# Kernel tuning notes

Measured on AMD Instinct MI355X. Metric: run time of the kernel, lower is better.

## Reference

```python
import jax, jax.numpy as jnp
import numpy as np

MARGIN = 0.3
BIG = 10000.0  # sentinel used by the original when a gt/lt negative set is empty


def setup_inputs() -> dict:
    key = jax.random.key(0)
    k1, k2 = jax.random.split(key)
    inputs = jax.random.normal(k1, (4096, 256), dtype=jnp.float32)
    targets = jax.random.randint(k2, (4096,), 0, 4, dtype=jnp.int32)
    return {"inputs": inputs, "targets": targets}


def reference(inputs, targets):
    # Pairwise Euclidean distance matrix (n, n).
    sq = jnp.sum(inputs * inputs, axis=1)
    d2 = sq[:, None] + sq[None, :] - 2.0 * (inputs @ inputs.T)
    dist = jnp.sqrt(jnp.maximum(d2, 0.0))

    # mask[i, j] semantics from the torch code (rows of expand are `targets`):
    #   eq: targets[j] == targets[i]; gt: targets[j] > targets[i]; lt: targets[j] < targets[i]
    eq = targets[None, :] == targets[:, None]
    gt = targets[None, :] > targets[:, None]
    lt = targets[None, :] < targets[:, None]

    # Hardest positive: max distance over same-label columns (diag always eq -> non-empty).
    hard_ap = jnp.max(jnp.where(eq, dist, -jnp.inf), axis=1)
    # Hardest greater / less negatives: min distance, sentinel BIG when set empty.
    an_g = jnp.min(jnp.where(gt, dist, jnp.inf), axis=1)
    an_g = jnp.where(jnp.isinf(an_g), BIG, an_g)
    an_l = jnp.min(jnp.where(lt, dist, jnp.inf), axis=1)
    an_l = jnp.where(jnp.isinf(an_l), BIG, an_l)

    loss = jnp.mean(jax.nn.relu(hard_ap - jnp.abs(an_g - an_l) + MARGIN))
    # cnt: rows whose positive set is just the anchor itself
    cnt = jnp.sum(jnp.sum(eq, axis=1) == 1)
    return loss, dist, cnt
```

## Files before the change

kernel.cpp:

```cpp
#include <hip/hip_runtime.h>

#define N 4096
#define D 256
#define MARGIN 0.3f
#define BIG 10000.0f

typedef _Float16 f16x8 __attribute__((ext_vector_type(8)));
typedef _Float16 f16x4 __attribute__((ext_vector_type(4)));
typedef float floatx16 __attribute__((ext_vector_type(16)));

__device__ inline void atomicMaxFloatPos(float* a, float v) {
    atomicMax((int*)a, __float_as_int(v));
}
__device__ inline void atomicMinFloatPos(float* a, float v) {
    atomicMin((int*)a, __float_as_int(v));
}

__device__ inline void gl_lds16(const void* g, void* l) {
    __builtin_amdgcn_global_load_lds(
        (const __attribute__((address_space(1))) unsigned int*)g,
        (__attribute__((address_space(3))) unsigned int*)l, 16, 0, 0);
}

__global__ __launch_bounds__(256) void prep_kernel(const float* __restrict__ x,
                                                   float* __restrict__ sq,
                                                   _Float16* __restrict__ Xf,
                                                   float* ap, float* ang, float* anl) {
    const int wave = threadIdx.x >> 6, lane = threadIdx.x & 63;
    const int row = blockIdx.x * 4 + wave;
    const float4 v = *(const float4*)(x + (size_t)row * D + lane * 4);
    f16x4 h;
    h[0] = (_Float16)v.x; h[1] = (_Float16)v.y;
    h[2] = (_Float16)v.z; h[3] = (_Float16)v.w;
    *(f16x4*)(Xf + (size_t)row * D + lane * 4) = h;
    const float c0 = (float)h[0], c1 = (float)h[1], c2 = (float)h[2], c3 = (float)h[3];
    float s = c0 * c0 + c1 * c1 + c2 * c2 + c3 * c3;
    #pragma unroll
    for (int off = 32; off; off >>= 1) s += __shfl_down(s, off);
    if (lane == 0) sq[row] = s;
    if (threadIdx.x < 4) {
        const int i = blockIdx.x * 4 + threadIdx.x;
        ap[i] = 0.0f; ang[i] = BIG; anl[i] = BIG;
    }
}

__global__ __launch_bounds__(64) void dist_kernel(const _Float16* __restrict__ Xf,
                                                  const int* __restrict__ tgt,
                                                  const float* __restrict__ sq,
                                                  float* __restrict__ dist,
                                                  float* ap, float* ang, float* anl) {
    __shared__ _Float16 lds[8192];
    _Float16* ldsA = lds;
    _Float16* ldsB = lds + 4096;
    float*    ldsC = (float*)lds;

    const int lane = threadIdx.x;
    const int row0 = blockIdx.y * 64;
    const int col0 = blockIdx.x * 64;

    const int drow = lane >> 3;
    const int q    = (lane & 7) ^ drow;

    floatx16 acc[2][2];
    #pragma unroll
    for (int mt = 0; mt < 2; ++mt)
        #pragma unroll
        for (int nt = 0; nt < 2; ++nt)
            #pragma unroll
            for (int r = 0; r < 16; ++r) acc[mt][nt][r] = 0.0f;

    const int m0 = lane & 31;
    const int m1 = 32 + m0;

    for (int s = 0; s < 4; ++s) {
        const int k0 = s * 64;
        __asm__ volatile("s_waitcnt lgkmcnt(0)" ::: "memory");
        #pragma unroll
        for (int d = 0; d < 8; ++d) {
            const int r = d * 8 + drow;
            gl_lds16(Xf + (size_t)(row0 + r) * D + k0 + q * 8, ldsA + d * 512);
            gl_lds16(Xf + (size_t)(col0 + r) * D + k0 + q * 8, ldsB + d * 512);
        }
        __asm__ volatile("s_waitcnt vmcnt(0)" ::: "memory");

        #pragma unroll
        for (int ks = 0; ks < 4; ++ks) {
            const int lq = ks * 2 + (lane >> 5);
            f16x8 a0 = *(const f16x8*)(ldsA + m0 * 64 + ((lq ^ (m0 & 7)) << 3));
            f16x8 a1 = *(const f16x8*)(ldsA + m1 * 64 + ((lq ^ (m1 & 7)) << 3));
            f16x8 b0 = *(const f16x8*)(ldsB + m0 * 64 + ((lq ^ (m0 & 7)) << 3));
            f16x8 b1 = *(const f16x8*)(ldsB + m1 * 64 + ((lq ^ (m1 & 7)) << 3));
            acc[0][0] = __builtin_amdgcn_mfma_f32_32x32x16_f16(a0, b0, acc[0][0], 0, 0, 0);
            acc[0][1] = __builtin_amdgcn_mfma_f32_32x32x16_f16(a0, b1, acc[0][1], 0, 0, 0);
            acc[1][0] = __builtin_amdgcn_mfma_f32_32x32x16_f16(a1, b0, acc[1][0], 0, 0, 0);
            acc[1][1] = __builtin_amdgcn_mfma_f32_32x32x16_f16(a1, b1, acc[1][1], 0, 0, 0);
        }
        __asm__ volatile("" ::: "memory");
    }

    const int gc0 = col0 + m0, gc1 = col0 + 32 + m0;
    const float sqc0 = sq[gc0], sqc1 = sq[gc1];
    const int rl_base = 4 * (lane >> 5);

    #pragma unroll
    for (int mt = 0; mt < 2; ++mt) {
        #pragma unroll
        for (int r = 0; r < 16; ++r) {
            const int row_l = mt * 32 + (r & 3) + 8 * (r >> 2) + rl_base;
            const int grow  = row0 + row_l;
            const float sqi = sq[grow];
            const float d0 = sqrtf(fmaxf(sqi + sqc0 - 2.0f * acc[mt][0][r], 0.0f));
            const float d1 = sqrtf(fmaxf(sqi + sqc1 - 2.0f * acc[mt][1][r], 0.0f));
            dist[(size_t)grow * N + gc0] = d0;
            dist[(size_t)grow * N + gc1] = d1;
            const int sw = row_l & 15;
            ldsC[row_l * 64 + (((m0 >> 2) ^ sw) << 2) + (m0 & 3)] = d0;
            ldsC[row_l * 64 + ((((m0 + 32) >> 2) ^ sw) << 2) + (m0 & 3)] = d1;
        }
    }
    __asm__ volatile("s_waitcnt lgkmcnt(0)" ::: "memory");

    const int grow = row0 + lane;
    const int ti   = tgt[grow];
    float mx = 0.0f, mg = BIG, ml = BIG;
    #pragma unroll
    for (int j = 0; j < 16; ++j) {
        const int4  t4 = *(const int4*)&tgt[col0 + j * 4];
        const float4 d4 = *(const float4*)&ldsC[lane * 64 + ((j ^ (lane & 15)) << 2)];
        if (t4.x == ti) mx = fmaxf(mx, d4.x); else if (t4.x > ti) mg = fminf(mg, d4.x); else ml = fminf(ml, d4.x);
        if (t4.y == ti) mx = fmaxf(mx, d4.y); else if (t4.y > ti) mg = fminf(mg, d4.y); else ml = fminf(ml, d4.y);
        if (t4.z == ti) mx = fmaxf(mx, d4.z); else if (t4.z > ti) mg = fminf(mg, d4.z); else ml = fminf(ml, d4.z);
        if (t4.w == ti) mx = fmaxf(mx, d4.w); else if (t4.w > ti) mg = fminf(mg, d4.w); else ml = fminf(ml, d4.w);
    }
    atomicMaxFloatPos(&ap[grow], mx);
    atomicMinFloatPos(&ang[grow], mg);
    atomicMinFloatPos(&anl[grow], ml);
}

__global__ __launch_bounds__(1024) void finish_kernel(const float* __restrict__ ap,
                                                      const float* __restrict__ ang,
                                                      const float* __restrict__ anl,
                                                      const int* __restrict__ tgt,
                                                      float* __restrict__ out) {
    __shared__ int hist[4];
    __shared__ unsigned hsum[2][16];
    __shared__ float wsum[16];
    __shared__ int wcnt[16];
    const int tid = threadIdx.x, lane = tid & 63, wv = tid >> 6;

    const int4 t4 = *(const int4*)&tgt[tid * 4];
    int c[4] = {0, 0, 0, 0};
    c[t4.x & 3]++; c[t4.y & 3]++; c[t4.z & 3]++; c[t4.w & 3]++;
    unsigned p01 = (unsigned)c[0] | ((unsigned)c[1] << 16);
    unsigned p23 = (unsigned)c[2] | ((unsigned)c[3] << 16);
    #pragma unroll
    for (int off = 32; off; off >>= 1) {
        p01 += __shfl_down(p01, off);
        p23 += __shfl_down(p23, off);
    }
    if (lane == 0) { hsum[0][wv] = p01; hsum[1][wv] = p23; }
    __syncthreads();
    if (tid == 0) {
        unsigned a = 0, b = 0;
        for (int i = 0; i < 16; ++i) { a += hsum[0][i]; b += hsum[1][i]; }
        hist[0] = a & 0xFFFF; hist[1] = a >> 16;
        hist[2] = b & 0xFFFF; hist[3] = b >> 16;
    }
    __syncthreads();

    float term = 0.0f; int cc = 0;
    const int lab[4] = {t4.x & 3, t4.y & 3, t4.z & 3, t4.w & 3};
    #pragma unroll
    for (int j = 0; j < 4; ++j) {
        const int i = tid * 4 + j;
        term += fmaxf(ap[i] - fabsf(ang[i] - anl[i]) + MARGIN, 0.0f);
        cc += (hist[lab[j]] == 1) ? 1 : 0;
    }
    #pragma unroll
    for (int off = 32; off; off >>= 1) {
        term += __shfl_down(term, off);
        cc   += __shfl_down(cc, off);
    }
    if (lane == 0) { wsum[wv] = term; wcnt[wv] = cc; }
    __syncthreads();
    if (tid == 0) {
        float ls = 0.0f; int cs = 0;
        for (int i = 0; i < 16; ++i) { ls += wsum[i]; cs += wcnt[i]; }
        out[0] = ls * (1.0f / N);
        out[1 + (size_t)N * N] = (float)cs;
    }
}

extern "C" void kernel_launch(void* const* d_in, const int* in_sizes, int n_in,
                              void* d_out, int out_size, void* d_ws, size_t ws_size,
                              hipStream_t stream) {
    const float* x   = (const float*)d_in[0];
    const int*   tgt = (const int*)d_in[1];
    float* out = (float*)d_out;
    char*  ws  = (char*)d_ws;

    _Float16* Xf  = (_Float16*)ws;
    float*    sq  = (float*)(ws + 2097152);
    float*    ap  = sq + 4096;
    float*    ang = sq + 8192;
    float*    anl = sq + 12288;

    prep_kernel<<<N / 4, 256, 0, stream>>>(x, sq, Xf, ap, ang, anl);
    dim3 grid(N / 64, N / 64);
    dist_kernel<<<grid, 64, 0, stream>>>(Xf, tgt, sq, out + 1, ap, ang, anl);
    finish_kernel<<<1, 1024, 0, stream>>>(ap, ang, anl, tgt, out);
}
```

Measured before the change: 114.6 us.

## Double-buffer global-to-LDS tile loads in distance GEMM kernel

Splits the LDS staging area into two A/B buffer pairs and unrolls the four K-steps. The next K-slice's global_load_lds is issued before computing on the current one, using partial vmcnt waits. This overlaps global memory latency with MFMA work inside each single-wave block, which previously waited for every load before computing. In exchange, LDS per block doubles, which can lower the number of resident blocks per CU. Buffer reuse also relies on the LDS reads of the previous compute finishing before the next load overwrites them.

```diff
diff --git a/kernel.cpp b/kernel.cpp
--- a/kernel.cpp
+++ b/kernel.cpp
@@ -49,9 +49,11 @@
                                                   const float* __restrict__ sq,
                                                   float* __restrict__ dist,
                                                   float* ap, float* ang, float* anl) {
-    __shared__ _Float16 lds[8192];
-    _Float16* ldsA = lds;
-    _Float16* ldsB = lds + 4096;
+    __shared__ _Float16 lds[16384];
+    _Float16* A0 = lds;
+    _Float16* B0 = lds + 4096;
+    _Float16* A1 = lds + 8192;
+    _Float16* B1 = lds + 12288;
     float*    ldsC = (float*)lds;
 
     const int lane = threadIdx.x;
@@ -60,6 +62,38 @@
 
     const int drow = lane >> 3;
     const int q    = (lane & 7) ^ drow;
+    const _Float16* gA = Xf + (size_t)(row0 + drow) * D + q * 8;
+    const _Float16* gB = Xf + (size_t)(col0 + drow) * D + q * 8;
+
+    const int m0 = lane & 31;
+    const int m1 = 32 + m0;
+
+    #define ISSUE(k0, la, lb)                                             \
+        {                                                                 \
+            _Pragma("unroll")                                             \
+            for (int d = 0; d < 8; ++d) {                                 \
+                gl_lds16(gA + (size_t)d * 8 * D + (k0), (la) + d * 512);  \
+                gl_lds16(gB + (size_t)d * 8 * D + (k0), (lb) + d * 512);  \
+            }                                                             \
+        }
+
+    #define COMPUTE(la, lb)                                                            \
+        {                                                                              \
+            _Pragma("unroll")                                                          \
+            for (int ks = 0; ks < 4; ++ks) {                                           \
+                const int lq = ks * 2 + (lane >> 5);                                   \
+                f16x8 a0 = *(const f16x8*)((la) + m0 * 64 + ((lq ^ (m0 & 7)) << 3));   \
+                f16x8 a1 = *(const f16x8*)((la) + m1 * 64 + ((lq ^ (m1 & 7)) << 3));   \
+                f16x8 b0 = *(const f16x8*)((lb) + m0 * 64 + ((lq ^ (m0 & 7)) << 3));   \
+                f16x8 b1 = *(const f16x8*)((lb) + m1 * 64 + ((lq ^ (m1 & 7)) << 3));   \
+                acc[0][0] = __builtin_amdgcn_mfma_f32_32x32x16_f16(a0, b0, acc[0][0], 0, 0, 0); \
+                acc[0][1] = __builtin_amdgcn_mfma_f32_32x32x16_f16(a0, b1, acc[0][1], 0, 0, 0); \
+                acc[1][0] = __builtin_amdgcn_mfma_f32_32x32x16_f16(a1, b0, acc[1][0], 0, 0, 0); \
+                acc[1][1] = __builtin_amdgcn_mfma_f32_32x32x16_f16(a1, b1, acc[1][1], 0, 0, 0); \
+            }                                                                          \
+        }
+
+    ISSUE(0, A0, B0);
 
     floatx16 acc[2][2];
     #pragma unroll
@@ -69,34 +103,17 @@
             #pragma unroll
             for (int r = 0; r < 16; ++r) acc[mt][nt][r] = 0.0f;
 
-    const int m0 = lane & 31;
-    const int m1 = 32 + m0;
-
-    for (int s = 0; s < 4; ++s) {
-        const int k0 = s * 64;
-        __asm__ volatile("s_waitcnt lgkmcnt(0)" ::: "memory");
-        #pragma unroll
-        for (int d = 0; d < 8; ++d) {
-            const int r = d * 8 + drow;
-            gl_lds16(Xf + (size_t)(row0 + r) * D + k0 + q * 8, ldsA + d * 512);
-            gl_lds16(Xf + (size_t)(col0 + r) * D + k0 + q * 8, ldsB + d * 512);
-        }
-        __asm__ volatile("s_waitcnt vmcnt(0)" ::: "memory");
-
-        #pragma unroll
-        for (int ks = 0; ks < 4; ++ks) {
-            const int lq = ks * 2 + (lane >> 5);
-            f16x8 a0 = *(const f16x8*)(ldsA + m0 * 64 + ((lq ^ (m0 & 7)) << 3));
-            f16x8 a1 = *(const f16x8*)(ldsA + m1 * 64 + ((lq ^ (m1 & 7)) << 3));
-            f16x8 b0 = *(const f16x8*)(ldsB + m0 * 64 + ((lq ^ (m0 & 7)) << 3));
-            f16x8 b1 = *(const f16x8*)(ldsB + m1 * 64 + ((lq ^ (m1 & 7)) << 3));
-            acc[0][0] = __builtin_amdgcn_mfma_f32_32x32x16_f16(a0, b0, acc[0][0], 0, 0, 0);
-            acc[0][1] = __builtin_amdgcn_mfma_f32_32x32x16_f16(a0, b1, acc[0][1], 0, 0, 0);
-            acc[1][0] = __builtin_amdgcn_mfma_f32_32x32x16_f16(a1, b0, acc[1][0], 0, 0, 0);
-            acc[1][1] = __builtin_amdgcn_mfma_f32_32x32x16_f16(a1, b1, acc[1][1], 0, 0, 0);
-        }
-        __asm__ volatile("" ::: "memory");
-    }
+    ISSUE(64, A1, B1);
+    __asm__ volatile("s_waitcnt vmcnt(16)" ::: "memory");
+    COMPUTE(A0, B0);
+    ISSUE(128, A0, B0);
+    __asm__ volatile("s_waitcnt vmcnt(16)" ::: "memory");
+    COMPUTE(A1, B1);
+    ISSUE(192, A1, B1);
+    __asm__ volatile("s_waitcnt vmcnt(16)" ::: "memory");
+    COMPUTE(A0, B0);
+    __asm__ volatile("s_waitcnt vmcnt(0)" ::: "memory");
+    COMPUTE(A1, B1);
 
     const int gc0 = col0 + m0, gc1 = col0 + 32 + m0;
     const float sqc0 = sq[gc0], sqc1 = sq[gc1];
@@ -135,6 +152,8 @@
     atomicMaxFloatPos(&ap[grow], mx);
     atomicMinFloatPos(&ang[grow], mg);
     atomicMinFloatPos(&anl[grow], ml);
+    #undef ISSUE
+    #undef COMPUTE
 }
 
 __global__ __launch_bounds__(1024) void finish_kernel(const float* __restrict__ ap,
```

Result: slower. 131.1 us (+14.3%).

## Load MFMA operands directly from global, reduce per row via shuffles, fuse finish

Applied to the files above, without the earlier changes.

Drops the LDS staging of the A/B tiles and loads f16x8 operands straight from global memory into the MFMA inputs. The per-row max/min reduction now runs in registers with cross-lane shuffles and atomics, with no LDS round trip. The finish kernel is folded into the last block, found through a global atomic counter. This removes LDS traffic and one launch, but adds many shuffles and atomics per row, uncoalesced global loads, and a single-wave serial tail.

```diff
diff --git a/kernel.cpp b/kernel.cpp
--- a/kernel.cpp
+++ b/kernel.cpp
@@ -4,6 +4,7 @@
 #define D 256
 #define MARGIN 0.3f
 #define BIG 10000.0f
+#define NBLK 4096
 
 typedef _Float16 f16x8 __attribute__((ext_vector_type(8)));
 typedef _Float16 f16x4 __attribute__((ext_vector_type(4)));
@@ -16,16 +17,11 @@
     atomicMin((int*)a, __float_as_int(v));
 }
 
-__device__ inline void gl_lds16(const void* g, void* l) {
-    __builtin_amdgcn_global_load_lds(
-        (const __attribute__((address_space(1))) unsigned int*)g,
-        (__attribute__((address_space(3))) unsigned int*)l, 16, 0, 0);
-}
-
 __global__ __launch_bounds__(256) void prep_kernel(const float* __restrict__ x,
                                                    float* __restrict__ sq,
                                                    _Float16* __restrict__ Xf,
-                                                   float* ap, float* ang, float* anl) {
+                                                   float* ap, float* ang, float* anl,
+                                                   unsigned* counter) {
     const int wave = threadIdx.x >> 6, lane = threadIdx.x & 63;
     const int row = blockIdx.x * 4 + wave;
     const float4 v = *(const float4*)(x + (size_t)row * D + lane * 4);
@@ -42,24 +38,26 @@
         const int i = blockIdx.x * 4 + threadIdx.x;
         ap[i] = 0.0f; ang[i] = BIG; anl[i] = BIG;
     }
+    if (blockIdx.x == 0 && threadIdx.x == 0) *counter = 0u;
 }
 
-__global__ __launch_bounds__(64) void dist_kernel(const _Float16* __restrict__ Xf,
-                                                  const int* __restrict__ tgt,
-                                                  const float* __restrict__ sq,
-                                                  float* __restrict__ dist,
-                                                  float* ap, float* ang, float* anl) {
-    __shared__ _Float16 lds[8192];
-    _Float16* ldsA = lds;
-    _Float16* ldsB = lds + 4096;
-    float*    ldsC = (float*)lds;
-
+__global__ __launch_bounds__(64, 3) void dist_kernel(const _Float16* __restrict__ Xf,
+                                                     const int* __restrict__ tgt,
+                                                     const float* __restrict__ sq,
+                                                     float* __restrict__ dist,
+                                                     float* ap, float* ang, float* anl,
+                                                     unsigned* counter,
+                                                     float* __restrict__ out) {
     const int lane = threadIdx.x;
     const int row0 = blockIdx.y * 64;
     const int col0 = blockIdx.x * 64;
 
-    const int drow = lane >> 3;
-    const int q    = (lane & 7) ^ drow;
+    const int ar = lane & 31;
+    const int kh = (lane >> 5) * 8;
+    const _Float16* pa0 = Xf + (size_t)(row0 + ar) * D + kh;
+    const _Float16* pa1 = pa0 + (size_t)32 * D;
+    const _Float16* pb0 = Xf + (size_t)(col0 + ar) * D + kh;
+    const _Float16* pb1 = pb0 + (size_t)32 * D;
 
     floatx16 acc[2][2];
     #pragma unroll
@@ -69,37 +67,21 @@
             #pragma unroll
             for (int r = 0; r < 16; ++r) acc[mt][nt][r] = 0.0f;
 
-    const int m0 = lane & 31;
-    const int m1 = 32 + m0;
-
-    for (int s = 0; s < 4; ++s) {
-        const int k0 = s * 64;
-        __asm__ volatile("s_waitcnt lgkmcnt(0)" ::: "memory");
-        #pragma unroll
-        for (int d = 0; d < 8; ++d) {
-            const int r = d * 8 + drow;
-            gl_lds16(Xf + (size_t)(row0 + r) * D + k0 + q * 8, ldsA + d * 512);
-            gl_lds16(Xf + (size_t)(col0 + r) * D + k0 + q * 8, ldsB + d * 512);
-        }
-        __asm__ volatile("s_waitcnt vmcnt(0)" ::: "memory");
-
-        #pragma unroll
-        for (int ks = 0; ks < 4; ++ks) {
-            const int lq = ks * 2 + (lane >> 5);
-            f16x8 a0 = *(const f16x8*)(ldsA + m0 * 64 + ((lq ^ (m0 & 7)) << 3));
-            f16x8 a1 = *(const f16x8*)(ldsA + m1 * 64 + ((lq ^ (m1 & 7)) << 3));
-            f16x8 b0 = *(const f16x8*)(ldsB + m0 * 64 + ((lq ^ (m0 & 7)) << 3));
-            f16x8 b1 = *(const f16x8*)(ldsB + m1 * 64 + ((lq ^ (m1 & 7)) << 3));
-            acc[0][0] = __builtin_amdgcn_mfma_f32_32x32x16_f16(a0, b0, acc[0][0], 0, 0, 0);
-            acc[0][1] = __builtin_amdgcn_mfma_f32_32x32x16_f16(a0, b1, acc[0][1], 0, 0, 0);
-            acc[1][0] = __builtin_amdgcn_mfma_f32_32x32x16_f16(a1, b0, acc[1][0], 0, 0, 0);
-            acc[1][1] = __builtin_amdgcn_mfma_f32_32x32x16_f16(a1, b1, acc[1][1], 0, 0, 0);
-        }
-        __asm__ volatile("" ::: "memory");
+    #pragma unroll
+    for (int ks = 0; ks < 16; ++ks) {
+        const f16x8 a0 = *(const f16x8*)(pa0 + ks * 16);
+        const f16x8 a1 = *(const f16x8*)(pa1 + ks * 16);
+        const f16x8 b0 = *(const f16x8*)(pb0 + ks * 16);
+        const f16x8 b1 = *(const f16x8*)(pb1 + ks * 16);
+        acc[0][0] = __builtin_amdgcn_mfma_f32_32x32x16_f16(a0, b0, acc[0][0], 0, 0, 0);
+        acc[0][1] = __builtin_amdgcn_mfma_f32_32x32x16_f16(a0, b1, acc[0][1], 0, 0, 0);
+        acc[1][0] = __builtin_amdgcn_mfma_f32_32x32x16_f16(a1, b0, acc[1][0], 0, 0, 0);
+        acc[1][1] = __builtin_amdgcn_mfma_f32_32x32x16_f16(a1, b1, acc[1][1], 0, 0, 0);
     }
 
-    const int gc0 = col0 + m0, gc1 = col0 + 32 + m0;
+    const int gc0 = col0 + ar, gc1 = col0 + 32 + ar;
     const float sqc0 = sq[gc0], sqc1 = sq[gc1];
+    const int tc0 = tgt[gc0], tc1 = tgt[gc1];
     const int rl_base = 4 * (lane >> 5);
 
     #pragma unroll
@@ -109,85 +91,67 @@
             const int row_l = mt * 32 + (r & 3) + 8 * (r >> 2) + rl_base;
             const int grow  = row0 + row_l;
             const float sqi = sq[grow];
+            const int   ti  = tgt[grow];
             const float d0 = sqrtf(fmaxf(sqi + sqc0 - 2.0f * acc[mt][0][r], 0.0f));
             const float d1 = sqrtf(fmaxf(sqi + sqc1 - 2.0f * acc[mt][1][r], 0.0f));
             dist[(size_t)grow * N + gc0] = d0;
             dist[(size_t)grow * N + gc1] = d1;
-            const int sw = row_l & 15;
-            ldsC[row_l * 64 + (((m0 >> 2) ^ sw) << 2) + (m0 & 3)] = d0;
-            ldsC[row_l * 64 + ((((m0 + 32) >> 2) ^ sw) << 2) + (m0 & 3)] = d1;
+            float mx = 0.0f, mg = BIG, ml = BIG;
+            if (tc0 == ti)      mx = d0;
+            else if (tc0 > ti)  mg = d0;
+            else                ml = d0;
+            if (tc1 == ti)      mx = fmaxf(mx, d1);
+            else if (tc1 > ti)  mg = fminf(mg, d1);
+            else                ml = fminf(ml, d1);
+            #pragma unroll
+            for (int off = 1; off < 32; off <<= 1) {
+                mx = fmaxf(mx, __shfl_xor(mx, off, 32));
+                mg = fminf(mg, __shfl_xor(mg, off, 32));
+                ml = fminf(ml, __shfl_xor(ml, off, 32));
+            }
+            if (ar == 0) {
+                atomicMaxFloatPos(&ap[grow], mx);
+                atomicMinFloatPos(&ang[grow], mg);
+                atomicMinFloatPos(&anl[grow], ml);
+            }
         }
     }
-    __asm__ volatile("s_waitcnt lgkmcnt(0)" ::: "memory");
 
-    const int grow = row0 + lane;
-    const int ti   = tgt[grow];
-    float mx = 0.0f, mg = BIG, ml = BIG;
-    #pragma unroll
-    for (int j = 0; j < 16; ++j) {
-        const int4  t4 = *(const int4*)&tgt[col0 + j * 4];
-        const float4 d4 = *(const float4*)&ldsC[lane * 64 + ((j ^ (lane & 15)) << 2)];
-        if (t4.x == ti) mx = fmaxf(mx, d4.x); else if (t4.x > ti) mg = fminf(mg, d4.x); else ml = fminf(ml, d4.x);
-        if (t4.y == ti) mx = fmaxf(mx, d4.y); else if (t4.y > ti) mg = fminf(mg, d4.y); else ml = fminf(ml, d4.y);
-        if (t4.z == ti) mx = fmaxf(mx, d4.z); else if (t4.z > ti) mg = fminf(mg, d4.z); else ml = fminf(ml, d4.z);
-        if (t4.w == ti) mx = fmaxf(mx, d4.w); else if (t4.w > ti) mg = fminf(mg, d4.w); else ml = fminf(ml, d4.w);
+    __threadfence();
+    unsigned done = 0;
+    if (lane == 0) done = atomicAdd(counter, 1u);
+    done = __shfl(done, 0);
+    if (done != NBLK - 1) return;
+    __threadfence();
+
+    int c0 = 0, c1 = 0, c2 = 0, c3 = 0;
+    #pragma unroll 4
+    for (int j = 0; j < 64; ++j) {
+        const int lab = tgt[j * 64 + lane] & 3;
+        c0 += (lab == 0); c1 += (lab == 1); c2 += (lab == 2); c3 += (lab == 3);
     }
-    atomicMaxFloatPos(&ap[grow], mx);
-    atomicMinFloatPos(&ang[grow], mg);
-    atomicMinFloatPos(&anl[grow], ml);
-}
-
-__global__ __launch_bounds__(1024) void finish_kernel(const float* __restrict__ ap,
-                                                      const float* __restrict__ ang,
-                                                      const float* __restrict__ anl,
-                                                      const int* __restrict__ tgt,
-                                                      float* __restrict__ out) {
-    __shared__ int hist[4];
-    __shared__ unsigned hsum[2][16];
-    __shared__ float wsum[16];
-    __shared__ int wcnt[16];
-    const int tid = threadIdx.x, lane = tid & 63, wv = tid >> 6;
-
-    const int4 t4 = *(const int4*)&tgt[tid * 4];
-    int c[4] = {0, 0, 0, 0};
-    c[t4.x & 3]++; c[t4.y & 3]++; c[t4.z & 3]++; c[t4.w & 3]++;
-    unsigned p01 = (unsigned)c[0] | ((unsigned)c[1] << 16);
-    unsigned p23 = (unsigned)c[2] | ((unsigned)c[3] << 16);
     #pragma unroll
     for (int off = 32; off; off >>= 1) {
-        p01 += __shfl_down(p01, off);
-        p23 += __shfl_down(p23, off);
+        c0 += __shfl_xor(c0, off); c1 += __shfl_xor(c1, off);
+        c2 += __shfl_xor(c2, off); c3 += __shfl_xor(c3, off);
     }
-    if (lane == 0) { hsum[0][wv] = p01; hsum[1][wv] = p23; }
-    __syncthreads();
-    if (tid == 0) {
-        unsigned a = 0, b = 0;
-        for (int i = 0; i < 16; ++i) { a += hsum[0][i]; b += hsum[1][i]; }
-        hist[0] = a & 0xFFFF; hist[1] = a >> 16;
-        hist[2] = b & 0xFFFF; hist[3] = b >> 16;
-    }
-    __syncthreads();
+    const int hist[4] = {c0, c1, c2, c3};
 
     float term = 0.0f; int cc = 0;
-    const int lab[4] = {t4.x & 3, t4.y & 3, t4.z & 3, t4.w & 3};
-    #pragma unroll
-    for (int j = 0; j < 4; ++j) {
-        const int i = tid * 4 + j;
+    #pragma unroll 4
+    for (int j = 0; j < 64; ++j) {
+        const int i = j * 64 + lane;
         term += fmaxf(ap[i] - fabsf(ang[i] - anl[i]) + MARGIN, 0.0f);
-        cc += (hist[lab[j]] == 1) ? 1 : 0;
+        cc += (hist[tgt[i] & 3] == 1) ? 1 : 0;
     }
     #pragma unroll
     for (int off = 32; off; off >>= 1) {
         term += __shfl_down(term, off);
         cc   += __shfl_down(cc, off);
     }
-    if (lane == 0) { wsum[wv] = term; wcnt[wv] = cc; }
-    __syncthreads();
-    if (tid == 0) {
-        float ls = 0.0f; int cs = 0;
-        for (int i = 0; i < 16; ++i) { ls += wsum[i]; cs += wcnt[i]; }
-        out[0] = ls * (1.0f / N);
-        out[1 + (size_t)N * N] = (float)cs;
+    if (lane == 0) {
+        out[0] = term * (1.0f / N);
+        out[1 + (size_t)N * N] = (float)cc;
     }
 }
 
@@ -204,9 +168,9 @@
     float*    ap  = sq + 4096;
     float*    ang = sq + 8192;
     float*    anl = sq + 12288;
+    unsigned* cnt = (unsigned*)(sq + 16384);
 
-    prep_kernel<<<N / 4, 256, 0, stream>>>(x, sq, Xf, ap, ang, anl);
+    prep_kernel<<<N / 4, 256, 0, stream>>>(x, sq, Xf, ap, ang, anl, cnt);
     dim3 grid(N / 64, N / 64);
-    dist_kernel<<<grid, 64, 0, stream>>>(Xf, tgt, sq, out + 1, ap, ang, anl);
-    finish_kernel<<<1, 1024, 0, stream>>>(ap, ang, anl, tgt, out);
+    dist_kernel<<<grid, 64, 0, stream>>>(Xf, tgt, sq, out + 1, ap, ang, anl, cnt, out);
 }
```

Measured after the change: 266.7 us. +132.6%, slower.
